# Performance work log

Hardware: AMD Instinct MI355X
Metric: run time of the kernel (lower is better)

## Reference

```python
import jax, jax.numpy as jnp
import numpy as np
import math

HIDDEN = 1024
N_HEADS = 16
HEAD = HIDDEN // N_HEADS
NEG_INF = -10000.0


def setup_inputs() -> dict:
    key = jax.random.key(0)
    ks = jax.random.split(key, 5)
    B, S = 4, 2048
    x = jax.random.normal(ks[0], (B, S, HIDDEN), dtype=jnp.float32)
    sc = 1.0 / math.sqrt(HIDDEN)
    qkv_w = jax.random.normal(ks[1], (HIDDEN, 3 * HIDDEN), dtype=jnp.float32) * sc
    qkv_b = jnp.zeros((3 * HIDDEN,), dtype=jnp.float32)
    out_w = jax.random.normal(ks[2], (HIDDEN, HIDDEN), dtype=jnp.float32) * sc
    out_b = jnp.zeros((HIDDEN,), dtype=jnp.float32)
    return {"x": x, "qkv_w": qkv_w, "qkv_b": qkv_b, "out_w": out_w, "out_b": out_b}


def reference(x, qkv_w, qkv_b, out_w, out_b):
    B, S, H = x.shape
    qkv = x @ qkv_w + qkv_b                      # [B,S,3H]
    q, k, v = jnp.split(qkv, 3, axis=-1)
    # b n (h l) -> b h n l
    def heads(t):
        return t.reshape(B, S, N_HEADS, HEAD).transpose(0, 2, 1, 3)
    q, k, v = heads(q), heads(k), heads(v)
    scores = jnp.einsum('bhql,bhkl->bhqk', q, k) / math.sqrt(HEAD)
    q_ind = jnp.arange(S)[:, None]
    k_ind = jnp.arange(S)[None, :]
    mask = q_ind < k_ind                          # future positions
    scores = jnp.where(mask, NEG_INF, scores)
    attn = jax.nn.softmax(scores, axis=-1)
    ctx = jnp.einsum('bhqk,bhkl->bhql', attn, v)  # [B,H,S,l]
    ctx = ctx.transpose(0, 2, 1, 3).reshape(B, S, H)
    return ctx @ out_w + out_b
```

## Files before the change

### kernel.cpp

```cpp
#include <hip/hip_runtime.h>

#define HIDDEN 1024
#define NHEADS 16
#define HEAD   64
#define BATCH  4
#define SEQ    2048
#define BS     (BATCH*SEQ)
#define H3     (3*HIDDEN)

typedef unsigned short u16;
typedef unsigned int   u32;
typedef __bf16 bf16x8 __attribute__((ext_vector_type(8)));
typedef float  f32x4  __attribute__((ext_vector_type(4)));

__device__ __forceinline__ u16 f2bf(float f) {
    union { float f; u32 u; } v; v.f = f;
    u32 u = v.u;
    u32 r = u + 0x7FFFu + ((u >> 16) & 1u);
    return (u16)(r >> 16);
}

__device__ __forceinline__ u16 f2bf_n(float f) {
    __bf16 h = (__bf16)f;
    union { __bf16 h; u16 u; } v; v.h = h;
    return v.u;
}

__device__ __forceinline__ void gload_lds16(const u16* g, u16* l) {
    __builtin_amdgcn_global_load_lds(
        (const __attribute__((address_space(1))) void*)g,
        (__attribute__((address_space(3))) void*)l, 16, 0, 0);
}

__global__ __launch_bounds__(256) void conv_x(
    const float* __restrict__ in, u16* __restrict__ out)
{
    const size_t i = ((size_t)blockIdx.x * 256 + threadIdx.x) * 8;
    float4 v0 = *(const float4*)&in[i];
    float4 v1 = *(const float4*)&in[i + 4];
    u16 u[8];
    u[0]=f2bf(v0.x); u[1]=f2bf(v0.y); u[2]=f2bf(v0.z); u[3]=f2bf(v0.w);
    u[4]=f2bf(v1.x); u[5]=f2bf(v1.y); u[6]=f2bf(v1.z); u[7]=f2bf(v1.w);
    *(uint4*)&out[i] = *(uint4*)u;
}

__global__ __launch_bounds__(256) void conv_wt(
    const float* __restrict__ w, u16* __restrict__ wt, int N)
{
    __shared__ float tile[64][65];
    const int t  = threadIdx.x;
    const int n0 = blockIdx.x * 64;
    const int k0 = blockIdx.y * 64;
#pragma unroll
    for (int i = 0; i < 4; i++) {
        int kr = i * 16 + (t >> 4);
        int c4 = (t & 15) * 4;
        float4 v = *(const float4*)&w[(size_t)(k0 + kr) * N + n0 + c4];
        tile[kr][c4+0] = v.x; tile[kr][c4+1] = v.y;
        tile[kr][c4+2] = v.z; tile[kr][c4+3] = v.w;
    }
    __syncthreads();
#pragma unroll
    for (int i = 0; i < 4; i++) {
        int nr = i * 16 + (t >> 4);
        int k4 = (t & 15) * 4;
        ushort4 uu;
        uu.x = f2bf(tile[k4+0][nr]); uu.y = f2bf(tile[k4+1][nr]);
        uu.z = f2bf(tile[k4+2][nr]); uu.w = f2bf(tile[k4+3][nr]);
        *(ushort4*)&wt[(size_t)(n0 + nr) * 1024 + k0 + k4] = uu;
    }
}

__global__ __launch_bounds__(256) void qkv_gemm(
    const u16* __restrict__ A, const u16* __restrict__ Bt,
    const float* __restrict__ bias,
    u16* __restrict__ q_ws, u16* __restrict__ k_ws, u16* __restrict__ vt_ws)
{
    __shared__ u16 a_lds[128 * 64];
    __shared__ u16 b_lds[128 * 64];

    const int swz    = (blockIdx.x & 7) * 192 + (blockIdx.x >> 3);
    const int m0     = (swz / 24) * 128;
    const int n0     = (swz % 24) * 128;

    const int t    = threadIdx.x;
    const int lane = t & 63, wv = t >> 6;
    const int lr   = lane & 15, lg = lane >> 4;
    const int wr   = wv >> 1, wc = wv & 1;
    const int srow = wv * 32 + (lane >> 3);
    const int sseg = (lane & 7) * 8;

    f32x4 acc[4][4];
#pragma unroll
    for (int m = 0; m < 4; m++)
#pragma unroll
        for (int n = 0; n < 4; n++)
#pragma unroll
            for (int r = 0; r < 4; r++) acc[m][n][r] = 0.f;

    for (int kt = 0; kt < 16; kt++) {
        const int kk = kt * 64;
        __syncthreads();
#pragma unroll
        for (int i = 0; i < 4; i++) {
            int row = srow + i * 8;
            gload_lds16(&A [(size_t)(m0 + row) * 1024 + kk + sseg], &a_lds[row * 64 + sseg]);
            gload_lds16(&Bt[(size_t)(n0 + row) * 1024 + kk + sseg], &b_lds[row * 64 + sseg]);
        }
        __syncthreads();

        bf16x8 af[2][4], bf[2][4];
#pragma unroll
        for (int ks = 0; ks < 2; ks++) {
#pragma unroll
            for (int m = 0; m < 4; m++)
                af[ks][m] = *(const bf16x8*)&a_lds[(wr * 64 + m * 16 + lr) * 64 + ks * 32 + lg * 8];
#pragma unroll
            for (int n = 0; n < 4; n++)
                bf[ks][n] = *(const bf16x8*)&b_lds[(wc * 64 + n * 16 + lr) * 64 + ks * 32 + lg * 8];
        }
#pragma unroll
        for (int ks = 0; ks < 2; ks++)
#pragma unroll
            for (int m = 0; m < 4; m++)
#pragma unroll
                for (int n = 0; n < 4; n++)
                    acc[m][n] = __builtin_amdgcn_mfma_f32_16x16x32_bf16(af[ks][m], bf[ks][n], acc[m][n], 0, 0, 0);
    }

#pragma unroll
    for (int m = 0; m < 4; m++) {
#pragma unroll
        for (int n = 0; n < 4; n++) {
#pragma unroll
            for (int r = 0; r < 4; r++) {
                int row = m0 + wr * 64 + m * 16 + lg * 4 + r;
                int col = n0 + wc * 64 + n * 16 + lr;
                float val = acc[m][n][r] + bias[col];
                int which = col >> 10;
                int cid   = col & 1023;
                int h = cid >> 6, d = cid & 63;
                int b = row >> 11, s = row & 2047;
                int bh = b * NHEADS + h;
                if (which == 0)
                    q_ws[((size_t)bh * SEQ + s) * HEAD + d] = f2bf(val * 0.125f);
                else if (which == 1)
                    k_ws[((size_t)bh * SEQ + s) * HEAD + d] = f2bf(val);
                else
                    vt_ws[((size_t)bh * HEAD + d) * SEQ + s] = f2bf(val);
            }
        }
    }
}

__global__ __launch_bounds__(256) void out_gemm(
    const u16* __restrict__ A, const u16* __restrict__ Bt,
    const float* __restrict__ bias, float* __restrict__ out)
{
    __shared__ u16 a_lds[128 * 64];
    __shared__ u16 b_lds[128 * 64];

    const int swz = (blockIdx.x & 7) * 64 + (blockIdx.x >> 3);
    const int m0  = (swz >> 3) * 128;
    const int n0  = (swz & 7) * 128;

    const int t    = threadIdx.x;
    const int lane = t & 63, wv = t >> 6;
    const int lr   = lane & 15, lg = lane >> 4;
    const int wr   = wv >> 1, wc = wv & 1;
    const int srow = wv * 32 + (lane >> 3);
    const int sseg = (lane & 7) * 8;

    f32x4 acc[4][4];
#pragma unroll
    for (int m = 0; m < 4; m++)
#pragma unroll
        for (int n = 0; n < 4; n++)
#pragma unroll
            for (int r = 0; r < 4; r++) acc[m][n][r] = 0.f;

    for (int kt = 0; kt < 16; kt++) {
        const int kk = kt * 64;
        __syncthreads();
#pragma unroll
        for (int i = 0; i < 4; i++) {
            int row = srow + i * 8;
            gload_lds16(&A [(size_t)(m0 + row) * 1024 + kk + sseg], &a_lds[row * 64 + sseg]);
            gload_lds16(&Bt[(size_t)(n0 + row) * 1024 + kk + sseg], &b_lds[row * 64 + sseg]);
        }
        __syncthreads();

        bf16x8 af[2][4], bf[2][4];
#pragma unroll
        for (int ks = 0; ks < 2; ks++) {
#pragma unroll
            for (int m = 0; m < 4; m++)
                af[ks][m] = *(const bf16x8*)&a_lds[(wr * 64 + m * 16 + lr) * 64 + ks * 32 + lg * 8];
#pragma unroll
            for (int n = 0; n < 4; n++)
                bf[ks][n] = *(const bf16x8*)&b_lds[(wc * 64 + n * 16 + lr) * 64 + ks * 32 + lg * 8];
        }
#pragma unroll
        for (int ks = 0; ks < 2; ks++)
#pragma unroll
            for (int m = 0; m < 4; m++)
#pragma unroll
                for (int n = 0; n < 4; n++)
                    acc[m][n] = __builtin_amdgcn_mfma_f32_16x16x32_bf16(af[ks][m], bf[ks][n], acc[m][n], 0, 0, 0);
    }

#pragma unroll
    for (int m = 0; m < 4; m++) {
#pragma unroll
        for (int n = 0; n < 4; n++) {
#pragma unroll
            for (int r = 0; r < 4; r++) {
                int row = m0 + wr * 64 + m * 16 + lg * 4 + r;
                int col = n0 + wc * 64 + n * 16 + lr;
                out[(size_t)row * HIDDEN + col] = acc[m][n][r] + bias[col];
            }
        }
    }
}

__global__ __launch_bounds__(512) void attn_kernel(
    const u16* __restrict__ q_ws, const u16* __restrict__ k_ws,
    const u16* __restrict__ vt_ws, u16* __restrict__ ctx_ws)
{
    __shared__ u16 k_lds[2][64][72];
    __shared__ u16 vt_lds[2][64][72];
    __shared__ u16 p_lds[8][16][72];

    const int t  = threadIdx.x;
    const int g  = blockIdx.x;
    const int bh  = ((g >> 7) << 3) | (g & 7);
    const int qt2 = 15 - ((g >> 3) & 15);

    const int lane = t & 63, wv = t >> 6;
    const int lr   = lane & 15, lg = lane >> 4;
    const int srow = t >> 3;
    const int sseg = (t & 7) * 8;

    const u16* kbase = k_ws  + (size_t)bh * SEQ * HEAD;
    const u16* vbase = vt_ws + (size_t)bh * HEAD * SEQ;

    const int qr0 = qt2 * 128 + wv * 16;
    bf16x8 qa[2];
#pragma unroll
    for (int ks = 0; ks < 2; ks++)
        qa[ks] = *(const bf16x8*)&q_ws[((size_t)bh * SEQ + qr0 + lr) * HEAD + ks * 32 + lg * 8];

    {
        uint4 a0 = *(const uint4*)&kbase[(size_t)srow * HEAD + sseg];
        uint4 b0 = *(const uint4*)&vbase[(size_t)srow * SEQ + sseg];
        *(uint4*)&k_lds[0][srow][sseg]  = a0;
        *(uint4*)&vt_lds[0][srow][sseg] = b0;
    }
    __syncthreads();

    f32x4 acc_o[4];
#pragma unroll
    for (int df = 0; df < 4; df++)
#pragma unroll
        for (int r = 0; r < 4; r++) acc_o[df][r] = 0.f;
    float m_run[4], l_part[4];
#pragma unroll
    for (int r = 0; r < 4; r++) { m_run[r] = -3e38f; l_part[r] = 0.f; }

    int cur = 0;
    const int ktmax = 2 * qt2 + 1;
    for (int kt = 0; kt <= ktmax; kt++) {
        const bool pf = (kt < ktmax);
        uint4 kn, vn;
        if (pf) {
            kn = *(const uint4*)&kbase[(size_t)((kt + 1) * 64 + srow) * HEAD + sseg];
            vn = *(const uint4*)&vbase[(size_t)srow * SEQ + (kt + 1) * 64 + sseg];
        }

        if (kt * 64 <= qr0 + 15) {
            f32x4 s_acc[4];
#pragma unroll
            for (int nf = 0; nf < 4; nf++) {
#pragma unroll
                for (int r = 0; r < 4; r++) s_acc[nf][r] = 0.f;
#pragma unroll
                for (int ks = 0; ks < 2; ks++) {
                    bf16x8 kb = *(const bf16x8*)&k_lds[cur][nf * 16 + lr][ks * 32 + lg * 8];
                    s_acc[nf] = __builtin_amdgcn_mfma_f32_16x16x32_bf16(qa[ks], kb, s_acc[nf], 0, 0, 0);
                }
            }

            if (kt * 64 + 63 > qr0) {
#pragma unroll
                for (int nf = 0; nf < 4; nf++)
#pragma unroll
                    for (int r = 0; r < 4; r++) {
                        int gq = qr0 + lg * 4 + r;
                        int gk = kt * 64 + nf * 16 + lr;
                        if (gk > gq) s_acc[nf][r] = -1e9f;
                    }
            }

            float p[4][4];
#pragma unroll
            for (int r = 0; r < 4; r++) {
                float mx = fmaxf(fmaxf(s_acc[0][r], s_acc[1][r]), fmaxf(s_acc[2][r], s_acc[3][r]));
#pragma unroll
                for (int off = 8; off >= 1; off >>= 1)
                    mx = fmaxf(mx, __shfl_xor(mx, off));
                float m_new = fmaxf(m_run[r], mx);
                float sc = __expf(m_run[r] - m_new);
                float rs;
                p[0][r] = __expf(s_acc[0][r] - m_new);
                p[1][r] = __expf(s_acc[1][r] - m_new);
                p[2][r] = __expf(s_acc[2][r] - m_new);
                p[3][r] = __expf(s_acc[3][r] - m_new);
                rs = (p[0][r] + p[1][r]) + (p[2][r] + p[3][r]);
                l_part[r] = l_part[r] * sc + rs;
                m_run[r] = m_new;
#pragma unroll
                for (int df = 0; df < 4; df++) acc_o[df][r] *= sc;
            }

#pragma unroll
            for (int nf = 0; nf < 4; nf++)
#pragma unroll
                for (int r = 0; r < 4; r++)
                    p_lds[wv][lg * 4 + r][nf * 16 + lr] = f2bf_n(p[nf][r]);

            bf16x8 pa[2];
#pragma unroll
            for (int ks = 0; ks < 2; ks++)
                pa[ks] = *(const bf16x8*)&p_lds[wv][lr][ks * 32 + lg * 8];

#pragma unroll
            for (int df = 0; df < 4; df++) {
#pragma unroll
                for (int ks = 0; ks < 2; ks++) {
                    bf16x8 vb = *(const bf16x8*)&vt_lds[cur][df * 16 + lr][ks * 32 + lg * 8];
                    acc_o[df] = __builtin_amdgcn_mfma_f32_16x16x32_bf16(pa[ks], vb, acc_o[df], 0, 0, 0);
                }
            }
        }

        if (pf) {
            const int nxt = cur ^ 1;
            *(uint4*)&k_lds[nxt][srow][sseg]  = kn;
            *(uint4*)&vt_lds[nxt][srow][sseg] = vn;
            __syncthreads();
            cur = nxt;
        }
    }

    float inv[4];
#pragma unroll
    for (int r = 0; r < 4; r++) {
        float l = l_part[r];
#pragma unroll
        for (int off = 8; off >= 1; off >>= 1)
            l += __shfl_xor(l, off);
        inv[r] = 1.f / l;
    }

    const int b = bh >> 4, h = bh & 15;
#pragma unroll
    for (int r = 0; r < 4; r++) {
        int s = qr0 + lg * 4 + r;
#pragma unroll
        for (int df = 0; df < 4; df++) {
            int d = df * 16 + lr;
            ctx_ws[((size_t)(b * SEQ + s)) * HIDDEN + h * HEAD + d] = f2bf_n(acc_o[df][r] * inv[r]);
        }
    }
}

extern "C" void kernel_launch(void* const* d_in, const int* in_sizes, int n_in,
                              void* d_out, int out_size, void* d_ws, size_t ws_size,
                              hipStream_t stream)
{
    const float* x    = (const float*)d_in[0];
    const float* qkvw = (const float*)d_in[1];
    const float* qkvb = (const float*)d_in[2];
    const float* outw = (const float*)d_in[3];
    const float* outb = (const float*)d_in[4];
    float* out = (float*)d_out;

    const size_t per = (size_t)BATCH * NHEADS * SEQ * HEAD;
    u16* q_ws   = (u16*)d_ws;
    u16* k_ws   = q_ws + per;
    u16* vt_ws  = k_ws + per;
    u16* c_ws   = vt_ws + per;
    u16* xb     = c_ws + per;
    u16* wqkvt  = xb + per;
    u16* wot    = wqkvt + (size_t)H3 * HIDDEN;

    conv_x <<<dim3((BS * HIDDEN) / (256 * 8)), 256, 0, stream>>>(x, xb);
    conv_wt<<<dim3(H3 / 64, HIDDEN / 64), 256, 0, stream>>>(qkvw, wqkvt, H3);
    conv_wt<<<dim3(HIDDEN / 64, HIDDEN / 64), 256, 0, stream>>>(outw, wot, HIDDEN);

    qkv_gemm<<<dim3(64 * 24), 256, 0, stream>>>(xb, wqkvt, qkvb, q_ws, k_ws, vt_ws);
    attn_kernel<<<dim3(64 * 16), 512, 0, stream>>>(q_ws, k_ws, vt_ws, c_ws);
    out_gemm<<<dim3(64 * 8), 256, 0, stream>>>(c_ws, wot, outb, out);
}
```

Before: 351.0 us.

## Process two balanced query fragments per wave and add lazy softmax rescaling

Each attention block now covers 256 query rows instead of 128. Every wave handles two 16-row fragments chosen as mirrored pairs (one near the start and one near the end of the tile), so causal work is balanced across waves and each loaded K/V tile is reused for twice as many queries. The grid is halved to match. The online softmax now skips rescaling the accumulator unless the new row max exceeds the running max by more than 8, which cuts exp and multiply work. The P LDS padding also changes from 72 to 68. The cost is roughly double the per-wave register state (accumulators, Q fragments, max/sum), fewer blocks to fill the GPU, and possible exp overflow risk that the threshold is meant to bound.

```diff
diff --git a/kernel.cpp b/kernel.cpp
--- a/kernel.cpp
+++ b/kernel.cpp
@@ -229,12 +229,12 @@
 {
     __shared__ u16 k_lds[2][64][72];
     __shared__ u16 vt_lds[2][64][72];
-    __shared__ u16 p_lds[8][16][72];
+    __shared__ u16 p_lds[8][16][68];
 
     const int t  = threadIdx.x;
     const int g  = blockIdx.x;
-    const int bh  = ((g >> 7) << 3) | (g & 7);
-    const int qt2 = 15 - ((g >> 3) & 15);
+    const int bh = ((g >> 6) << 3) | (g & 7);
+    const int qt = 7 - ((g >> 3) & 7);
 
     const int lane = t & 63, wv = t >> 6;
     const int lr   = lane & 15, lg = lane >> 4;
@@ -244,11 +244,16 @@
     const u16* kbase = k_ws  + (size_t)bh * SEQ * HEAD;
     const u16* vbase = vt_ws + (size_t)bh * HEAD * SEQ;
 
-    const int qr0 = qt2 * 128 + wv * 16;
-    bf16x8 qa[2];
-#pragma unroll
-    for (int ks = 0; ks < 2; ks++)
-        qa[ks] = *(const bf16x8*)&q_ws[((size_t)bh * SEQ + qr0 + lr) * HEAD + ks * 32 + lg * 8];
+    int frow[2];
+    frow[0] = qt * 256 + wv * 16;
+    frow[1] = qt * 256 + 128 + (7 - wv) * 16;
+
+    bf16x8 qa[2][2];
+#pragma unroll
+    for (int f = 0; f < 2; f++)
+#pragma unroll
+        for (int ks = 0; ks < 2; ks++)
+            qa[f][ks] = *(const bf16x8*)&q_ws[((size_t)bh * SEQ + frow[f] + lr) * HEAD + ks * 32 + lg * 8];
 
     {
         uint4 a0 = *(const uint4*)&kbase[(size_t)srow * HEAD + sseg];
@@ -258,17 +263,21 @@
     }
     __syncthreads();
 
-    f32x4 acc_o[4];
-#pragma unroll
-    for (int df = 0; df < 4; df++)
-#pragma unroll
-        for (int r = 0; r < 4; r++) acc_o[df][r] = 0.f;
-    float m_run[4], l_part[4];
-#pragma unroll
-    for (int r = 0; r < 4; r++) { m_run[r] = -3e38f; l_part[r] = 0.f; }
+    f32x4 acc_o[2][4];
+#pragma unroll
+    for (int f = 0; f < 2; f++)
+#pragma unroll
+        for (int df = 0; df < 4; df++)
+#pragma unroll
+            for (int r = 0; r < 4; r++) acc_o[f][df][r] = 0.f;
+    float m_run[2][4], l_part[2][4];
+#pragma unroll
+    for (int f = 0; f < 2; f++)
+#pragma unroll
+        for (int r = 0; r < 4; r++) { m_run[f][r] = -3e38f; l_part[f][r] = 0.f; }
 
     int cur = 0;
-    const int ktmax = 2 * qt2 + 1;
+    const int ktmax = 4 * qt + 3;
     for (int kt = 0; kt <= ktmax; kt++) {
         const bool pf = (kt < ktmax);
         uint4 kn, vn;
@@ -277,7 +286,10 @@
             vn = *(const uint4*)&vbase[(size_t)srow * SEQ + (kt + 1) * 64 + sseg];
         }
 
-        if (kt * 64 <= qr0 + 15) {
+#pragma unroll
+        for (int f = 0; f < 2; f++) {
+            if (kt * 64 > frow[f] + 15) continue;
+
             f32x4 s_acc[4];
 #pragma unroll
             for (int nf = 0; nf < 4; nf++) {
@@ -286,40 +298,52 @@
 #pragma unroll
                 for (int ks = 0; ks < 2; ks++) {
                     bf16x8 kb = *(const bf16x8*)&k_lds[cur][nf * 16 + lr][ks * 32 + lg * 8];
-                    s_acc[nf] = __builtin_amdgcn_mfma_f32_16x16x32_bf16(qa[ks], kb, s_acc[nf], 0, 0, 0);
+                    s_acc[nf] = __builtin_amdgcn_mfma_f32_16x16x32_bf16(qa[f][ks], kb, s_acc[nf], 0, 0, 0);
                 }
             }
 
-            if (kt * 64 + 63 > qr0) {
+            if (kt * 64 + 63 > frow[f]) {
 #pragma unroll
                 for (int nf = 0; nf < 4; nf++)
 #pragma unroll
                     for (int r = 0; r < 4; r++) {
-                        int gq = qr0 + lg * 4 + r;
+                        int gq = frow[f] + lg * 4 + r;
                         int gk = kt * 64 + nf * 16 + lr;
                         if (gk > gq) s_acc[nf][r] = -1e9f;
                     }
             }
 
+            float mx[4];
+            bool need = false;
+#pragma unroll
+            for (int r = 0; r < 4; r++) {
+                float m = fmaxf(fmaxf(s_acc[0][r], s_acc[1][r]), fmaxf(s_acc[2][r], s_acc[3][r]));
+#pragma unroll
+                for (int off = 8; off >= 1; off >>= 1)
+                    m = fmaxf(m, __shfl_xor(m, off));
+                mx[r] = m;
+                need = need || (m > m_run[f][r] + 8.f);
+            }
+            if (__any(need)) {
+#pragma unroll
+                for (int r = 0; r < 4; r++) {
+                    float m_new = fmaxf(m_run[f][r], mx[r]);
+                    float sc = __expf(m_run[f][r] - m_new);
+                    l_part[f][r] *= sc;
+                    m_run[f][r] = m_new;
+#pragma unroll
+                    for (int df = 0; df < 4; df++) acc_o[f][df][r] *= sc;
+                }
+            }
+
             float p[4][4];
 #pragma unroll
             for (int r = 0; r < 4; r++) {
-                float mx = fmaxf(fmaxf(s_acc[0][r], s_acc[1][r]), fmaxf(s_acc[2][r], s_acc[3][r]));
-#pragma unroll
-                for (int off = 8; off >= 1; off >>= 1)
-                    mx = fmaxf(mx, __shfl_xor(mx, off));
-                float m_new = fmaxf(m_run[r], mx);
-                float sc = __expf(m_run[r] - m_new);
-                float rs;
-                p[0][r] = __expf(s_acc[0][r] - m_new);
-                p[1][r] = __expf(s_acc[1][r] - m_new);
-                p[2][r] = __expf(s_acc[2][r] - m_new);
-                p[3][r] = __expf(s_acc[3][r] - m_new);
-                rs = (p[0][r] + p[1][r]) + (p[2][r] + p[3][r]);
-                l_part[r] = l_part[r] * sc + rs;
-                m_run[r] = m_new;
-#pragma unroll
-                for (int df = 0; df < 4; df++) acc_o[df][r] *= sc;
+                p[0][r] = __expf(s_acc[0][r] - m_run[f][r]);
+                p[1][r] = __expf(s_acc[1][r] - m_run[f][r]);
+                p[2][r] = __expf(s_acc[2][r] - m_run[f][r]);
+                p[3][r] = __expf(s_acc[3][r] - m_run[f][r]);
+                l_part[f][r] += (p[0][r] + p[1][r]) + (p[2][r] + p[3][r]);
             }
 
 #pragma unroll
@@ -338,7 +362,7 @@
 #pragma unroll
                 for (int ks = 0; ks < 2; ks++) {
                     bf16x8 vb = *(const bf16x8*)&vt_lds[cur][df * 16 + lr][ks * 32 + lg * 8];
-                    acc_o[df] = __builtin_amdgcn_mfma_f32_16x16x32_bf16(pa[ks], vb, acc_o[df], 0, 0, 0);
+                    acc_o[f][df] = __builtin_amdgcn_mfma_f32_16x16x32_bf16(pa[ks], vb, acc_o[f][df], 0, 0, 0);
                 }
             }
         }
@@ -352,24 +376,22 @@
         }
     }
 
-    float inv[4];
-#pragma unroll
-    for (int r = 0; r < 4; r++) {
-        float l = l_part[r];
-#pragma unroll
-        for (int off = 8; off >= 1; off >>= 1)
-            l += __shfl_xor(l, off);
-        inv[r] = 1.f / l;
-    }
-
     const int b = bh >> 4, h = bh & 15;
 #pragma unroll
-    for (int r = 0; r < 4; r++) {
-        int s = qr0 + lg * 4 + r;
-#pragma unroll
-        for (int df = 0; df < 4; df++) {
-            int d = df * 16 + lr;
-            ctx_ws[((size_t)(b * SEQ + s)) * HIDDEN + h * HEAD + d] = f2bf_n(acc_o[df][r] * inv[r]);
+    for (int f = 0; f < 2; f++) {
+#pragma unroll
+        for (int r = 0; r < 4; r++) {
+            float l = l_part[f][r];
+#pragma unroll
+            for (int off = 8; off >= 1; off >>= 1)
+                l += __shfl_xor(l, off);
+            float inv = 1.f / l;
+            int s = frow[f] + lg * 4 + r;
+#pragma unroll
+            for (int df = 0; df < 4; df++) {
+                int d = df * 16 + lr;
+                ctx_ws[((size_t)(b * SEQ + s)) * HIDDEN + h * HEAD + d] = f2bf_n(acc_o[f][df][r] * inv);
+            }
         }
     }
 }
@@ -399,6 +421,6 @@
     conv_wt<<<dim3(HIDDEN / 64, HIDDEN / 64), 256, 0, stream>>>(outw, wot, HIDDEN);
 
     qkv_gemm<<<dim3(64 * 24), 256, 0, stream>>>(xb, wqkvt, qkvb, q_ws, k_ws, vt_ws);
-    attn_kernel<<<dim3(64 * 16), 512, 0, stream>>>(q_ws, k_ws, vt_ws, c_ws);
+    attn_kernel<<<dim3(64 * 8), 512, 0, stream>>>(q_ws, k_ws, vt_ws, c_ws);
     out_gemm<<<dim3(64 * 8), 256, 0, stream>>>(c_ws, wot, outb, out);
 }
```

Result: slower. 412.1 us (+17.4%).
